# Kernel tuning notes

Hardware: AMD Instinct MI355X
Metric: run time of the kernel (lower is better)

The kernel has to match this reference:

```python
import jax, jax.numpy as jnp
import numpy as np

C = 192
CR = C // 4  # reduced channels in attention bottleneck


def setup_inputs() -> dict:
    key = jax.random.key(0)
    k = jax.random.split(key, 6)
    x = jax.random.normal(k[0], (32, C, 16, 28, 28), dtype=jnp.float32)
    # Conv1d kernel_size=1 weights -> plain matrices
    w1 = jax.random.normal(k[1], (CR, C), dtype=jnp.float32) * (1.0 / np.sqrt(C))
    b1 = jax.random.normal(k[2], (CR,), dtype=jnp.float32) * 0.01
    w2 = jax.random.normal(k[3], (C, CR), dtype=jnp.float32) * (1.0 / np.sqrt(CR))
    b2 = jax.random.normal(k[4], (C,), dtype=jnp.float32) * 0.01
    scale_weights = jnp.array([0.5, 0.3, 0.2], dtype=jnp.float32)
    return {"x": x, "w1": w1, "b1": b1, "w2": w2, "b2": b2, "scale_weights": scale_weights}


def reference(x, w1, b1, w2, b2, scale_weights):
    # x: [B, C, T, H, W]
    B, Cc, T, H, W = x.shape
    # AdaptiveAvgPool3d((None,1,1)) -> mean over H,W: [B, C, T]
    squeezed = x.mean(axis=(3, 4))
    # 1x1 Conv1d bottleneck attention: sigmoid(W2 relu(W1 s + b1) + b2)
    h = jax.nn.relu(jnp.einsum('oc,bct->bot', w1, squeezed) + b1[None, :, None])
    attn = jax.nn.sigmoid(jnp.einsum('co,bot->bct', w2, h) + b2[None, :, None])
    # attention-weighted temporal sum: [B, C, H, W]
    attended = jnp.einsum('bcthw,bct->bchw', x, attn)
    recent = x[:, :, -1]                      # last frame
    mid = x[:, :, T // 2:].mean(axis=2)       # second half mean
    overall = x.mean(axis=2)                  # full mean
    w = jax.nn.softmax(scale_weights)
    multi_scale = w[0] * recent + w[1] * mid + w[2] * overall
    return 0.5 * attended + 0.5 * multi_scale
```

## Files before the change

kernel.cpp:

```cpp
#include <hip/hip_runtime.h>
#include <math.h>

#define NB 32
#define NC 192
#define NCR 48
#define NT 16
#define NHW 784
#define NHW4 196

typedef float vfloat4 __attribute__((ext_vector_type(4)));

__global__ __launch_bounds__(256) void spatial_mean_kernel(
    const float* __restrict__ x, float* __restrict__ sq) {
  const int wave = threadIdx.x >> 6;
  const int lane = threadIdx.x & 63;
  const int slab = blockIdx.x * 4 + wave;
  const float4* x4 = (const float4*)x + (size_t)slab * NHW4;

  float s = 0.f;
  float4 v;
  v = x4[lane];        s += v.x + v.y + v.z + v.w;
  v = x4[lane + 64];   s += v.x + v.y + v.z + v.w;
  v = x4[lane + 128];  s += v.x + v.y + v.z + v.w;
  if (lane < 4) { v = x4[lane + 192]; s += v.x + v.y + v.z + v.w; }

  #pragma unroll
  for (int off = 32; off > 0; off >>= 1) s += __shfl_down(s, off);
  if (lane == 0) sq[slab] = s * (1.0f / (float)NHW);
}

__global__ __launch_bounds__(192) void attn_coef_kernel(
    const float* __restrict__ sq, const float* __restrict__ w1,
    const float* __restrict__ b1, const float* __restrict__ w2,
    const float* __restrict__ b2, const float* __restrict__ sw,
    float* __restrict__ coef) {
  __shared__ float s[NC];
  __shared__ float h[NCR];
  const int bt = blockIdx.x;
  const int b = bt >> 4;
  const int t = bt & 15;
  const int tid = threadIdx.x;

  s[tid] = sq[((b * NC + tid) * NT) + t];
  __syncthreads();

  if (tid < NCR) {
    float acc = b1[tid];
    const float* wr = w1 + tid * NC;
    #pragma unroll 8
    for (int c = 0; c < NC; ++c) acc += wr[c] * s[c];
    h[tid] = fmaxf(acc, 0.f);
  }
  __syncthreads();

  float acc = b2[tid];
  const float* wr = w2 + tid * NCR;
  #pragma unroll 8
  for (int o = 0; o < NCR; ++o) acc += wr[o] * h[o];
  const float attn = 1.f / (1.f + expf(-acc));

  const float s0 = sw[0], s1 = sw[1], s2 = sw[2];
  const float m = fmaxf(s0, fmaxf(s1, s2));
  const float e0 = expf(s0 - m), e1 = expf(s1 - m), e2 = expf(s2 - m);
  const float inv = 1.f / (e0 + e1 + e2);
  float ms = e2 * inv * (1.f / 16.f);
  if (t >= NT / 2) ms += e1 * inv * (1.f / 8.f);
  if (t == NT - 1) ms += e0 * inv;

  coef[(b * NC + tid) * NT + t] = 0.5f * attn + 0.5f * ms;
}

__global__ __launch_bounds__(256) void output_kernel(
    const float* __restrict__ x, const float* __restrict__ coef,
    float* __restrict__ out) {
  __shared__ float cf[NT];
  const int slab = (int)gridDim.x - 1 - (int)blockIdx.x;
  const int tid = threadIdx.x;

  if (tid < NT) cf[tid] = coef[slab * NT + tid];
  __syncthreads();

  if (tid < NHW4) {
    const vfloat4* x4 = (const vfloat4*)x + (size_t)slab * NT * NHW4 + tid;
    vfloat4 acc = {0.f, 0.f, 0.f, 0.f};
    #pragma unroll
    for (int t = 0; t < NT; ++t) {
      const vfloat4 v = __builtin_nontemporal_load(x4 + (size_t)t * NHW4);
      acc += v * cf[t];
    }
    __builtin_nontemporal_store(acc, (vfloat4*)out + (size_t)slab * NHW4 + tid);
  }
}

extern "C" void kernel_launch(void* const* d_in, const int* in_sizes, int n_in,
                              void* d_out, int out_size, void* d_ws, size_t ws_size,
                              hipStream_t stream) {
  const float* x  = (const float*)d_in[0];
  const float* w1 = (const float*)d_in[1];
  const float* b1 = (const float*)d_in[2];
  const float* w2 = (const float*)d_in[3];
  const float* b2 = (const float*)d_in[4];
  const float* sw = (const float*)d_in[5];
  float* out = (float*)d_out;

  float* sq   = (float*)d_ws;
  float* coef = sq + NB * NC * NT;

  spatial_mean_kernel<<<NB * NC * NT / 4, 256, 0, stream>>>(x, sq);
  attn_coef_kernel<<<NB * NT, 192, 0, stream>>>(sq, w1, b1, w2, b2, sw, coef);
  output_kernel<<<NB * NC, 256, 0, stream>>>(x, coef, out);
}
```

Before: 465.9 us.

## Pipeline batch groups so output pass of group g-1 overlaps mean pass of g

Splits the batch into four groups of eight and fuses the spatial-mean pass for group g with the weighted-sum output pass for group g-1 into one mixed launch, interleaving block roles one in five. The aim is to have x data for the next group read while the previous group's output is written, and to reuse L2/MALL residency: a group's x (about 77MB) may still be cached when re-read. The output loads switch from nontemporal to normal loads so that cached data can be used. The cost is more kernel launches and serial small attention launches between stages.

```diff
diff --git a/kernel.cpp b/kernel.cpp
--- a/kernel.cpp
+++ b/kernel.cpp
@@ -7,38 +7,74 @@
 #define NT 16
 #define NHW 784
 #define NHW4 196
+#define GB 8
+#define NGRP (NB / GB)
+#define SLABS_G (GB * NC * NT)
+#define BLKA (SLABS_G / 4)
+#define BLKC (GB * NC)
 
 typedef float vfloat4 __attribute__((ext_vector_type(4)));
 
-__global__ __launch_bounds__(256) void spatial_mean_kernel(
-    const float* __restrict__ x, float* __restrict__ sq) {
-  const int wave = threadIdx.x >> 6;
-  const int lane = threadIdx.x & 63;
-  const int slab = blockIdx.x * 4 + wave;
-  const float4* x4 = (const float4*)x + (size_t)slab * NHW4;
+__global__ __launch_bounds__(256) void pipe_kernel(
+    const float* __restrict__ x, float* __restrict__ sq,
+    const float* __restrict__ coef, float* __restrict__ out,
+    const int a_group, const int c_group, const int mixed) {
+  int ai = -1, ci = -1;
+  {
+    const int bx = (int)blockIdx.x;
+    if (mixed) {
+      if (bx % 5 == 0) ci = bx / 5;
+      else             ai = bx - bx / 5 - 1;
+    } else if (a_group >= 0) {
+      ai = bx;
+    } else {
+      ci = bx;
+    }
+  }
 
-  float s = 0.f;
-  float4 v;
-  v = x4[lane];        s += v.x + v.y + v.z + v.w;
-  v = x4[lane + 64];   s += v.x + v.y + v.z + v.w;
-  v = x4[lane + 128];  s += v.x + v.y + v.z + v.w;
-  if (lane < 4) { v = x4[lane + 192]; s += v.x + v.y + v.z + v.w; }
+  if (ai >= 0) {
+    const int wave = threadIdx.x >> 6;
+    const int lane = threadIdx.x & 63;
+    const int slab = a_group * SLABS_G + ai * 4 + wave;
+    const float4* x4 = (const float4*)x + (size_t)slab * NHW4;
 
-  #pragma unroll
-  for (int off = 32; off > 0; off >>= 1) s += __shfl_down(s, off);
-  if (lane == 0) sq[slab] = s * (1.0f / (float)NHW);
+    float s = 0.f;
+    float4 v;
+    v = x4[lane];        s += v.x + v.y + v.z + v.w;
+    v = x4[lane + 64];   s += v.x + v.y + v.z + v.w;
+    v = x4[lane + 128];  s += v.x + v.y + v.z + v.w;
+    if (lane < 4) { v = x4[lane + 192]; s += v.x + v.y + v.z + v.w; }
+
+    #pragma unroll
+    for (int off = 32; off > 0; off >>= 1) s += __shfl_down(s, off);
+    if (lane == 0) sq[slab] = s * (1.0f / (float)NHW);
+  } else {
+    __shared__ float cf[NT];
+    const int slab = c_group * BLKC + ci;
+    const int tid = threadIdx.x;
+
+    if (tid < NT) cf[tid] = coef[slab * NT + tid];
+    __syncthreads();
+
+    if (tid < NHW4) {
+      const vfloat4* x4 = (const vfloat4*)x + (size_t)slab * NT * NHW4 + tid;
+      vfloat4 acc = {0.f, 0.f, 0.f, 0.f};
+      #pragma unroll
+      for (int t = 0; t < NT; ++t) acc += x4[(size_t)t * NHW4] * cf[t];
+      __builtin_nontemporal_store(acc, (vfloat4*)out + (size_t)slab * NHW4 + tid);
+    }
+  }
 }
 
 __global__ __launch_bounds__(192) void attn_coef_kernel(
     const float* __restrict__ sq, const float* __restrict__ w1,
     const float* __restrict__ b1, const float* __restrict__ w2,
     const float* __restrict__ b2, const float* __restrict__ sw,
-    float* __restrict__ coef) {
+    float* __restrict__ coef, const int g) {
   __shared__ float s[NC];
   __shared__ float h[NCR];
-  const int bt = blockIdx.x;
-  const int b = bt >> 4;
-  const int t = bt & 15;
+  const int b = g * GB + ((int)blockIdx.x >> 4);
+  const int t = (int)blockIdx.x & 15;
   const int tid = threadIdx.x;
 
   s[tid] = sq[((b * NC + tid) * NT) + t];
@@ -70,28 +106,6 @@
   coef[(b * NC + tid) * NT + t] = 0.5f * attn + 0.5f * ms;
 }
 
-__global__ __launch_bounds__(256) void output_kernel(
-    const float* __restrict__ x, const float* __restrict__ coef,
-    float* __restrict__ out) {
-  __shared__ float cf[NT];
-  const int slab = (int)gridDim.x - 1 - (int)blockIdx.x;
-  const int tid = threadIdx.x;
-
-  if (tid < NT) cf[tid] = coef[slab * NT + tid];
-  __syncthreads();
-
-  if (tid < NHW4) {
-    const vfloat4* x4 = (const vfloat4*)x + (size_t)slab * NT * NHW4 + tid;
-    vfloat4 acc = {0.f, 0.f, 0.f, 0.f};
-    #pragma unroll
-    for (int t = 0; t < NT; ++t) {
-      const vfloat4 v = __builtin_nontemporal_load(x4 + (size_t)t * NHW4);
-      acc += v * cf[t];
-    }
-    __builtin_nontemporal_store(acc, (vfloat4*)out + (size_t)slab * NHW4 + tid);
-  }
-}
-
 extern "C" void kernel_launch(void* const* d_in, const int* in_sizes, int n_in,
                               void* d_out, int out_size, void* d_ws, size_t ws_size,
                               hipStream_t stream) {
@@ -106,7 +120,11 @@
   float* sq   = (float*)d_ws;
   float* coef = sq + NB * NC * NT;
 
-  spatial_mean_kernel<<<NB * NC * NT / 4, 256, 0, stream>>>(x, sq);
-  attn_coef_kernel<<<NB * NT, 192, 0, stream>>>(sq, w1, b1, w2, b2, sw, coef);
-  output_kernel<<<NB * NC, 256, 0, stream>>>(x, coef, out);
+  pipe_kernel<<<BLKA, 256, 0, stream>>>(x, sq, coef, out, 0, -1, 0);
+  attn_coef_kernel<<<GB * NT, 192, 0, stream>>>(sq, w1, b1, w2, b2, sw, coef, 0);
+  for (int g = 1; g < NGRP; ++g) {
+    pipe_kernel<<<BLKA + BLKC, 256, 0, stream>>>(x, sq, coef, out, g, g - 1, 1);
+    attn_coef_kernel<<<GB * NT, 192, 0, stream>>>(sq, w1, b1, w2, b2, sw, coef, g);
+  }
+  pipe_kernel<<<BLKC, 256, 0, stream>>>(x, sq, coef, out, -1, NGRP - 1, 0);
 }
```

After: 476.8 us. +2.3%, slower.
